# Kernel optimization log

Measured on AMD Instinct MI355X. Metric: run time of the kernel, lower is better.

## Reference

```python
import jax, jax.numpy as jnp
import numpy as np
from jax import lax

TEMP = 20.0    # args.temp
ATT_WT = 0.5   # args.att_wt
EPS = 1e-12


def l2norm(x, axis):
    # torch F.normalize: x / max(||x||_2, eps)
    n = jnp.sqrt(jnp.sum(x * x, axis=axis, keepdims=True))
    return x / jnp.maximum(n, EPS)


def conv4d(x, w):
    """4D conv, padding=1, stride=1.
    x: [B,Cin,H1,W1,H2,W2], w: [Cout,Cin,3,3,3,3] -> [B,Cout,H1,W1,H2,W2].
    Decomposed as 9 fixed (di,dj) shifts over (H1,W1), each a 2D conv over (H2,W2).
    """
    B, Cin, H1, W1, H2, W2 = x.shape
    Cout = w.shape[0]
    xp = jnp.pad(x, ((0, 0), (0, 0), (1, 1), (1, 1), (0, 0), (0, 0)))
    out = jnp.zeros((B * H1 * W1, Cout, H2, W2), x.dtype)
    for di in range(3):
        for dj in range(3):
            xs = xp[:, :, di:di + H1, dj:dj + W1]                      # [B,Cin,H1,W1,H2,W2]
            xr = xs.transpose(0, 2, 3, 1, 4, 5).reshape(B * H1 * W1, Cin, H2, W2)
            out = out + lax.conv_general_dilated(
                xr, w[:, :, di, dj], (1, 1), 'SAME',
                dimension_numbers=('NCHW', 'OIHW', 'NCHW'))
    return out.reshape(B, H1, W1, Cout, H2, W2).transpose(0, 3, 1, 2, 4, 5)


def nc_stack(x, ws):
    for w in ws:
        x = jax.nn.relu(conv4d(x, w))
    return x


def neigh_consensus(corr, ws):
    # symmetric mode: conv(C) + perm(conv(perm(C)))
    ct = corr.transpose(0, 1, 4, 5, 2, 3)
    return nc_stack(corr, ws) + nc_stack(ct, ws).transpose(0, 1, 4, 5, 2, 3)


def setup_inputs() -> dict:
    key = jax.random.key(0)
    ks = jax.random.split(key, 7)
    L, B, C, h, w = 9, 2, 1024, 20, 20
    ch = 256
    return {
        'fq_feats': jax.random.normal(ks[0], (L, B, C, h, w), jnp.float32),
        'fs_feats': jax.random.normal(ks[1], (L, B, C, h, w), jnp.float32),
        'f_q': jax.random.normal(ks[2], (B, ch, h, w), jnp.float32),
        'f_s': jax.random.normal(ks[3], (B, ch, h, w), jnp.float32),
        'w1': jax.random.normal(ks[4], (10, 9, 3, 3, 3, 3), jnp.float32) * 0.1,
        'w2': jax.random.normal(ks[5], (10, 10, 3, 3, 3, 3), jnp.float32) * 0.1,
        'w3': jax.random.normal(ks[6], (1, 10, 3, 3, 3, 3), jnp.float32) * 0.1,
    }


def reference(fq_feats, fs_feats, f_q, f_s, w1, w2, w3):
    L, B, C, h, w = fq_feats.shape
    ch = f_q.shape[1]
    hw = h * w
    # per-level channel-wise L2 normalization -> cosine correlation volume
    fqn = l2norm(fq_feats, axis=2)
    fsn = l2norm(fs_feats, axis=2)
    # corr4d[b,l,i,j,k,m] = <fq[:, i,j], fs[:, k,m]>  -> [B, L, h, w, h, w]
    corr4d = jnp.einsum('lbcij,lbckm->blijkm', fqn, fsn)
    # neighbourhood-consensus matching net -> [B,1,h,w,h,w]
    c4 = neigh_consensus(corr4d, (w1, w2, w3))
    attn = jax.nn.softmax(c4.reshape(B, hw, hw) * TEMP, axis=-1)  # over support positions
    v = f_s.reshape(B, ch, hw)
    att_fq = jnp.einsum('bqs,bcs->bcq', attn, v).reshape(B, ch, h, w)
    fq = l2norm(f_q, axis=1) + l2norm(att_fq, axis=1) * ATT_WT
    return (fq, att_fq)
```

## Files before the change

### kernel.cpp

```cpp
#include <hip/hip_runtime.h>
#include <math.h>
#include <stddef.h>

#define L9   9
#define NB   2
#define CF   1024
#define HW   400
#define CH   256
#define TEMPF 20.0f
#define EPSF  1e-12f

typedef _Float16 half8 __attribute__((ext_vector_type(8)));
typedef float f32x4 __attribute__((ext_vector_type(4)));
typedef unsigned short ushort_t;

__global__ __launch_bounds__(256) void norm_partial2(const float* __restrict__ fq,
                                                     const float* __restrict__ fs,
                                                     float* __restrict__ partial2) {
    int chunk = blockIdx.x, lb = blockIdx.y, t = blockIdx.z;
    int tid = threadIdx.x;
    if (tid >= 200) return;
    int half = tid / 100, p4 = tid - half * 100;
    const float* src = (t == 0 ? fq : fs) + (size_t)lb * CF * HW + p4 * 4;
    int c0 = chunk * 64 + half;
    f32x4 acc = {};
    #pragma unroll 8
    for (int it = 0; it < 32; ++it) {
        const float4 v = *(const float4*)(src + (size_t)(c0 + it * 2) * HW);
        acc[0] = fmaf(v.x, v.x, acc[0]);
        acc[1] = fmaf(v.y, v.y, acc[1]);
        acc[2] = fmaf(v.z, v.z, acc[2]);
        acc[3] = fmaf(v.w, v.w, acc[3]);
    }
    float* dst = partial2 + ((size_t)((t * 18 + lb) * 32) + chunk * 2 + half) * HW + p4 * 4;
    *(f32x4*)dst = acc;
}

__global__ __launch_bounds__(256) void norm_finalize2(const float* __restrict__ partial2,
                                                      float* __restrict__ invn) {
    int idx = blockIdx.x * 256 + threadIdx.x;
    if (idx >= 2 * 18 * HW) return;
    int t_lb = idx / HW;
    int ij = idx - t_lb * HW;
    const float* p = partial2 + (size_t)t_lb * 32 * HW + ij;
    float ss = 0.f;
    #pragma unroll
    for (int c = 0; c < 32; ++c) ss += p[c * HW];
    invn[idx] = 1.0f / fmaxf(sqrtf(ss), EPSF);
}

__global__ __launch_bounds__(256) void transpose_f16(const float* __restrict__ fq,
                                                     const float* __restrict__ fs,
                                                     ushort_t* __restrict__ At,
                                                     ushort_t* __restrict__ Bt,
                                                     int lb_base) {
    __shared__ float tile[64][65];
    int z = blockIdx.z;
    int tsel = z / 9, li = z - tsel * 9;
    int lb = lb_base + li;
    const float* src = (tsel ? fs : fq) + (size_t)lb * CF * HW;
    ushort_t* dst = (tsel ? Bt : At) + (size_t)li * HW * CF;
    int c0 = blockIdx.x * 64, ij0 = blockIdx.y * 64;
    int tid = threadIdx.x;
    int cl = tid >> 6;
    int col = tid & 63;
    #pragma unroll
    for (int rr = 0; rr < 16; ++rr) {
        int c_local = rr * 4 + cl;
        int ij = ij0 + col;
        tile[c_local][col] = (ij < HW) ? src[(size_t)(c0 + c_local) * HW + ij] : 0.f;
    }
    __syncthreads();
    int cp = (tid & 31) * 2;
    int rowsel = tid >> 5;
    #pragma unroll
    for (int rr = 0; rr < 8; ++rr) {
        int ij_local = rr * 8 + rowsel;
        int ij = ij0 + ij_local;
        if (ij < HW) {
            union { _Float16 h; ushort_t u; } h0, h1;
            h0.h = (_Float16)tile[cp][ij_local];
            h1.h = (_Float16)tile[cp + 1][ij_local];
            ushort2 o; o.x = h0.u; o.y = h1.u;
            *(ushort2*)(dst + (size_t)ij * CF + c0 + cp) = o;
        }
    }
}

__global__ __launch_bounds__(256) void corr_gemm_mfma(const ushort_t* __restrict__ At,
                                                      const ushort_t* __restrict__ Bt,
                                                      const float* __restrict__ invn,
                                                      ushort_t* __restrict__ corr,
                                                      int lb_base) {
    __shared__ ushort_t As[64][72];
    __shared__ ushort_t Bs[64][72];
    int li = blockIdx.z, lb = lb_base + li;
    int l = lb >> 1, b = lb & 1;
    int i0 = blockIdx.y * 64, j0 = blockIdx.x * 64;
    int tid = threadIdx.x, lane = tid & 63, w = tid >> 6;
    int mw = (w >> 1) * 32, nw = (w & 1) * 32;
    f32x4 acc[2][2] = {};
    const ushort_t* Abase = At + (size_t)li * HW * CF;
    const ushort_t* Bbase = Bt + (size_t)li * HW * CF;

    for (int kt = 0; kt < 16; ++kt) {
        int c0 = kt * 64;
        __syncthreads();
        #pragma unroll
        for (int p = 0; p < 2; ++p) {
            int idx = tid + p * 256;
            int row = idx >> 3, c8 = idx & 7;
            uint4 va = make_uint4(0, 0, 0, 0), vb = make_uint4(0, 0, 0, 0);
            if (i0 + row < HW) va = *(const uint4*)(Abase + (size_t)(i0 + row) * CF + c0 + c8 * 8);
            if (j0 + row < HW) vb = *(const uint4*)(Bbase + (size_t)(j0 + row) * CF + c0 + c8 * 8);
            *(uint4*)&As[row][c8 * 8] = va;
            *(uint4*)&Bs[row][c8 * 8] = vb;
        }
        __syncthreads();
        #pragma unroll
        for (int ks = 0; ks < 2; ++ks) {
            int k0 = ks * 32 + (lane >> 4) * 8;
            half8 a0 = *(const half8*)&As[mw + (lane & 15)][k0];
            half8 a1 = *(const half8*)&As[mw + 16 + (lane & 15)][k0];
            half8 b0 = *(const half8*)&Bs[nw + (lane & 15)][k0];
            half8 b1 = *(const half8*)&Bs[nw + 16 + (lane & 15)][k0];
            acc[0][0] = __builtin_amdgcn_mfma_f32_16x16x32_f16(a0, b0, acc[0][0], 0, 0, 0);
            acc[0][1] = __builtin_amdgcn_mfma_f32_16x16x32_f16(a0, b1, acc[0][1], 0, 0, 0);
            acc[1][0] = __builtin_amdgcn_mfma_f32_16x16x32_f16(a1, b0, acc[1][0], 0, 0, 0);
            acc[1][1] = __builtin_amdgcn_mfma_f32_16x16x32_f16(a1, b1, acc[1][1], 0, 0, 0);
        }
    }
    int obase = (b * 9 + l) * HW;
    #pragma unroll
    for (int mi = 0; mi < 2; ++mi) {
        #pragma unroll
        for (int ni = 0; ni < 2; ++ni) {
            #pragma unroll
            for (int r = 0; r < 4; ++r) {
                int ij = i0 + mw + mi * 16 + (lane >> 4) * 4 + r;
                int km = j0 + nw + ni * 16 + (lane & 15);
                if (ij < HW && km < HW) {
                    union { _Float16 h; ushort_t u; } cv;
                    cv.h = (_Float16)(acc[mi][ni][r] * invn[lb * HW + ij] * invn[7200 + lb * HW + km]);
                    corr[(size_t)(obase + ij) * HW + km] = cv.u;
                }
            }
        }
    }
}

template <int CIN, int COUT, bool SWAP>
__global__ __launch_bounds__(256) void wprep7(const float* __restrict__ wt,
                                              ushort_t* __restrict__ wb) {
    constexpr int S = CIN * 9;
    constexpr int NCH = (S + 31) / 32;
    int idx = blockIdx.x * 256 + threadIdx.x;
    int total = NCH * 4608;
    if (idx >= total) return;
    int k = idx & 31, n = (idx >> 5) & 15, dd = (idx >> 9) % 9, ch = idx / 4608;
    int slot = ch * 32 + k;
    float v = 0.f;
    if (n < COUT && slot < S) {
        int ci = slot / 9, pl = slot - ci * 9;
        int di = pl / 3, dj = pl % 3, dk = dd / 3, dm = dd % 3;
        int widx = SWAP ? ((((n * CIN + ci) * 3 + dk) * 3 + dm) * 3 + di) * 3 + dj
                        : ((((n * CIN + ci) * 3 + di) * 3 + dj) * 3 + dk) * 3 + dm;
        v = wt[widx];
    }
    union { _Float16 h; ushort_t u; } cv; cv.h = (_Float16)v;
    wb[idx] = cv.u;
}

template <int CIN, int COUT, bool DUAL, bool OUTF16>
__global__ __launch_bounds__(256) void conv4d_v8(const ushort_t* __restrict__ inA,
                                                 const ushort_t* __restrict__ inB,
                                                 const ushort_t* __restrict__ wbA,
                                                 const ushort_t* __restrict__ wbB,
                                                 void* __restrict__ outA,
                                                 void* __restrict__ outB) {
    constexpr int S = CIN * 9;
    constexpr int NCH = (S + 31) / 32;
    __shared__ __align__(16) ushort_t Ah[484 * 40];
    const int b = blockIdx.y, ij = blockIdx.x;
    const int z = blockIdx.z;
    const ushort_t* in = (DUAL || z == 0) ? inA : inB;
    const ushort_t* wbS = (DUAL || z == 0) ? wbA : wbB;
    void* outS = (DUAL || z == 0) ? outA : outB;
    const int i = ij / 20, j = ij - (ij / 20) * 20;
    const int tid = threadIdx.x, wv = tid >> 6, lane = tid & 63;
    const int m16 = lane & 15, q4 = lane >> 4;

    for (int p = tid; p < 484 * 20; p += 256) ((uint*)Ah)[p] = 0;

    int baseh[7];
    #pragma unroll
    for (int s = 0; s < 7; ++s) {
        int t = wv + 4 * s;
        if (t < 25) {
            int km = t * 16 + m16;
            int kk = km / 20, mm = km - kk * 20;
            baseh[s] = (kk * 22 + mm) * 40 + q4 * 8;
        } else baseh[s] = 0;
    }
    f32x4 accA[7] = {};
    f32x4 accB[7] = {};

    const bool stager = tid < 200;
    const int km1 = 2 * tid;
    const int r1 = stager ? ((km1 / 20 + 1) * 22 + (km1 % 20) + 1) : 0;
    int hofs[9]; bool vld[9];
    #pragma unroll
    for (int pl = 0; pl < 9; ++pl) {
        int ii = i + pl / 3 - 1, jj = j + pl % 3 - 1;
        vld[pl] = (unsigned)ii < 20u && (unsigned)jj < 20u;
        hofs[pl] = (ii * 20 + jj) * HW + km1;
    }
    const ushort_t* in_b = in + (size_t)b * CIN * HW * HW;
    const int wbase = m16 * 32 + q4 * 8;

    uint pf[32];
    #pragma unroll
    for (int u = 0; u < 32; ++u) {
        int slot = u;
        if (slot < S) {
            int ci = slot / 9, pl = slot - ci * 9;
            pf[u] = (stager && vld[pl]) ? *(const uint*)(in_b + ci * (HW * HW) + hofs[pl]) : 0u;
        } else pf[u] = 0u;
    }
    __syncthreads();

    #pragma unroll
    for (int ch = 0; ch < NCH; ++ch) {
        if (stager) {
            #pragma unroll
            for (int g4 = 0; g4 < 8; ++g4) {
                uint lo0 = (pf[4 * g4] & 0xFFFFu) | (pf[4 * g4 + 1] << 16);
                uint lo1 = (pf[4 * g4 + 2] & 0xFFFFu) | (pf[4 * g4 + 3] << 16);
                uint hi0 = (pf[4 * g4] >> 16) | (pf[4 * g4 + 1] & 0xFFFF0000u);
                uint hi1 = (pf[4 * g4 + 2] >> 16) | (pf[4 * g4 + 3] & 0xFFFF0000u);
                uint2 wlo; wlo.x = lo0; wlo.y = lo1;
                uint2 whi; whi.x = hi0; whi.y = hi1;
                *(uint2*)&Ah[(size_t)r1 * 40 + 4 * g4] = wlo;
                *(uint2*)&Ah[(size_t)(r1 + 1) * 40 + 4 * g4] = whi;
            }
        }
        __syncthreads();
        if (ch + 1 < NCH) {
            #pragma unroll
            for (int u = 0; u < 32; ++u) {
                int slot = (ch + 1) * 32 + u;
                if (slot < S) {
                    int ci = slot / 9, pl = slot - ci * 9;
                    pf[u] = (stager && vld[pl]) ? *(const uint*)(in_b + ci * (HW * HW) + hofs[pl]) : 0u;
                } else pf[u] = 0u;
            }
        }
        #pragma unroll
        for (int dd = 0; dd < 9; ++dd) {
            half8 bfA = *(const half8*)(wbS + (ch * 9 + dd) * 512 + wbase);
            half8 bfB;
            if (DUAL) bfB = *(const half8*)(wbB + (ch * 9 + dd) * 512 + wbase);
            const int doff = ((dd / 3) * 22 + (dd % 3)) * 40;
            #pragma unroll
            for (int s = 0; s < 7; ++s) {
                if (wv + 4 * s < 25) {
                    half8 af = *(const half8*)(Ah + baseh[s] + doff);
                    accA[s] = __builtin_amdgcn_mfma_f32_16x16x32_f16(af, bfA, accA[s], 0, 0, 0);
                    if (DUAL) accB[s] = __builtin_amdgcn_mfma_f32_16x16x32_f16(af, bfB, accB[s], 0, 0, 0);
                }
            }
        }
        if (ch + 1 < NCH) __syncthreads();
    }

    const int co = m16;
    if (co < COUT) {
        #pragma unroll
        for (int s = 0; s < 7; ++s) {
            int t = wv + 4 * s;
            if (t < 25) {
                int km0 = t * 16 + q4 * 4;
                size_t o = ((size_t)(b * COUT + co) * HW + ij) * HW + km0;
                if (OUTF16) {
                    union { ushort_t us[4]; uint2 u2; } pk;
                    #pragma unroll
                    for (int r = 0; r < 4; ++r) {
                        union { _Float16 h; ushort_t u16; } cv;
                        cv.h = (_Float16)fmaxf(accA[s][r], 0.f);
                        pk.us[r] = cv.u16;
                    }
                    *(uint2*)((ushort_t*)outS + o) = pk.u2;
                    if (DUAL) {
                        #pragma unroll
                        for (int r = 0; r < 4; ++r) {
                            union { _Float16 h; ushort_t u16; } cv;
                            cv.h = (_Float16)fmaxf(accB[s][r], 0.f);
                            pk.us[r] = cv.u16;
                        }
                        *(uint2*)((ushort_t*)outB + o) = pk.u2;
                    }
                } else {
                    float* op = (float*)outS + o;
                    #pragma unroll
                    for (int r = 0; r < 4; ++r)
                        op[r] = fmaxf(accA[s][r], 0.f);
                }
            }
        }
    }
}

__global__ __launch_bounds__(256) void fs_prep(const float* __restrict__ f_s,
                                               ushort_t* __restrict__ fsh) {
    int idx = blockIdx.x * 256 + threadIdx.x;
    if (idx >= NB * CH * 416) return;
    int s = idx % 416, bc = idx / 416;
    float v = (s < HW) ? f_s[(size_t)bc * HW + s] : 0.f;
    union { _Float16 h; ushort_t u; } cv; cv.h = (_Float16)v;
    fsh[idx] = cv.u;
}

__global__ __launch_bounds__(256) void softmax_av_mfma2(const float* __restrict__ c4A,
                                                        const float* __restrict__ c4B,
                                                        const ushort_t* __restrict__ fsh,
                                                        float* __restrict__ att) {
    __shared__ ushort_t P[64 * 424];
    __shared__ float invl[64];
    const int b = blockIdx.z, qb = blockIdx.x * 64;
    const int tid = threadIdx.x, wv = tid >> 6, lane = tid & 63;
    const int m16 = lane & 15, q4 = lane >> 4;
    const int lane16 = lane & 15, rg4 = lane >> 4;

    #pragma unroll 1
    for (int rg = 0; rg < 4; ++rg) {
        const int ql = wv * 16 + rg * 4 + rg4;
        int q = qb + ql; if (q > HW - 1) q = HW - 1;
        const float* rowA = c4A + ((size_t)b * HW + q) * HW;
        const float* rowB = c4B + ((size_t)b * HW + q) * HW;
        float4 v4[7];
        #pragma unroll
        for (int k4 = 0; k4 < 6; ++k4) {
            float4 a4 = *(const float4*)(rowA + 64 * k4 + lane16 * 4);
            float4 b4 = *(const float4*)(rowB + 64 * k4 + lane16 * 4);
            v4[k4] = make_float4(a4.x + b4.x, a4.y + b4.y, a4.z + b4.z, a4.w + b4.w);
        }
        if (lane16 < 4) {
            float4 a4 = *(const float4*)(rowA + 384 + lane16 * 4);
            float4 b4 = *(const float4*)(rowB + 384 + lane16 * 4);
            v4[6] = make_float4(a4.x + b4.x, a4.y + b4.y, a4.z + b4.z, a4.w + b4.w);
        } else {
            v4[6] = make_float4(-1e30f, -1e30f, -1e30f, -1e30f);
        }
        float mx = -1e30f;
        #pragma unroll
        for (int k4 = 0; k4 < 7; ++k4)
            mx = fmaxf(mx, fmaxf(fmaxf(v4[k4].x, v4[k4].y), fmaxf(v4[k4].z, v4[k4].w)));
        #pragma unroll
        for (int off = 8; off; off >>= 1) mx = fmaxf(mx, __shfl_xor(mx, off, 16));
        float sum = 0.f;
        #pragma unroll
        for (int k4 = 0; k4 < 7; ++k4) {
            if (k4 == 6 && lane16 >= 4) break;
            float e0 = __expf(TEMPF * (v4[k4].x - mx));
            float e1 = __expf(TEMPF * (v4[k4].y - mx));
            float e2 = __expf(TEMPF * (v4[k4].z - mx));
            float e3 = __expf(TEMPF * (v4[k4].w - mx));
            sum += e0 + e1 + e2 + e3;
            union { ushort_t us[4]; uint2 u2; } pk;
            union { _Float16 h; ushort_t u16; } cv;
            cv.h = (_Float16)e0; pk.us[0] = cv.u16;
            cv.h = (_Float16)e1; pk.us[1] = cv.u16;
            cv.h = (_Float16)e2; pk.us[2] = cv.u16;
            cv.h = (_Float16)e3; pk.us[3] = cv.u16;
            *(uint2*)&P[(size_t)ql * 424 + 64 * k4 + lane16 * 4] = pk.u2;
        }
        if (lane16 >= 4 && lane16 < 10) {
            uint2 z2; z2.x = 0; z2.y = 0;
            *(uint2*)&P[(size_t)ql * 424 + 384 + lane16 * 4] = z2;
        }
        #pragma unroll
        for (int off = 8; off; off >>= 1) sum += __shfl_xor(sum, off, 16);
        if (lane16 == 0) invl[ql] = 1.0f / sum;
    }

    half8 afr[13];
    #pragma unroll
    for (int ks = 0; ks < 13; ++ks)
        afr[ks] = *(const half8*)&P[(size_t)(wv * 16 + m16) * 424 + ks * 32 + q4 * 8];
    const ushort_t* fb = fsh + (size_t)b * CH * 416;
    #pragma unroll
    for (int ntl = 0; ntl < 2; ++ntl) {
        const int nt = blockIdx.y * 2 + ntl;
        const int c = nt * 16 + m16;
        const ushort_t* fc = fb + (size_t)c * 416 + q4 * 8;
        f32x4 acc = {};
        #pragma unroll
        for (int ks = 0; ks < 13; ++ks) {
            half8 bf = *(const half8*)(fc + ks * 32);
            acc = __builtin_amdgcn_mfma_f32_16x16x32_f16(afr[ks], bf, acc, 0, 0, 0);
        }
        #pragma unroll
        for (int r = 0; r < 4; ++r) {
            int ql = wv * 16 + q4 * 4 + r;
            int q = qb + ql;
            if (q < HW)
                att[((size_t)b * CH + c) * HW + q] = acc[r] * invl[ql];
        }
    }
}

__global__ __launch_bounds__(256) void final_fq(const float* __restrict__ f_q,
                                                const float* __restrict__ att,
                                                float* __restrict__ out_fq) {
    __shared__ float red[256];
    int b = blockIdx.y, q = blockIdx.x;
    int tid = threadIdx.x;
    size_t idx = (size_t)(b * CH + tid) * HW + q;
    float f = f_q[idx];
    float a = att[idx];
    red[tid] = f * f;
    __syncthreads();
    for (int s = 128; s > 0; s >>= 1) {
        if (tid < s) red[tid] += red[tid + s];
        __syncthreads();
    }
    float invf = 1.0f / fmaxf(sqrtf(red[0]), EPSF);
    __syncthreads();
    red[tid] = a * a;
    __syncthreads();
    for (int s = 128; s > 0; s >>= 1) {
        if (tid < s) red[tid] += red[tid + s];
        __syncthreads();
    }
    float inva = 1.0f / fmaxf(sqrtf(red[0]), EPSF);
    out_fq[idx] = f * invf + 0.5f * a * inva;
}

extern "C" void kernel_launch(void* const* d_in, const int* in_sizes, int n_in,
                              void* d_out, int out_size, void* d_ws, size_t ws_size,
                              hipStream_t stream) {
    const float* fq_feats = (const float*)d_in[0];
    const float* fs_feats = (const float*)d_in[1];
    const float* f_q      = (const float*)d_in[2];
    const float* f_s      = (const float*)d_in[3];
    const float* w1       = (const float*)d_in[4];
    const float* w2       = (const float*)d_in[5];
    const float* w3       = (const float*)d_in[6];
    float* out = (float*)d_out;

    float* ws      = (float*)d_ws;
    float* wbuf    = ws;
    float* invn    = wbuf + 115200;
    float* corr    = invn + 14400;
    float* buf1    = corr + 2880000;
    float* buf2    = buf1 + 3200000;
    float* att     = out + 204800;

    float* partial2 = buf1;
    ushort_t* corr_h = (ushort_t*)corr;
    ushort_t* fsh    = (ushort_t*)(corr + 1440000);
    float* c4A = corr + 1600000;
    float* c4B = corr + 1920000;
    ushort_t* At = (ushort_t*)buf1;
    ushort_t* Bt = (ushort_t*)buf2;
    ushort_t* b1A = (ushort_t*)buf1;
    ushort_t* b1B = b1A + 3200000;
    ushort_t* b2A = (ushort_t*)buf2;
    ushort_t* b2B = b2A + 3200000;

    ushort_t* wb0   = (ushort_t*)wbuf;
    ushort_t* wbL1A = wb0;
    ushort_t* wbL1B = wb0 + 13824;
    ushort_t* wbL2A = wb0 + 27648;
    ushort_t* wbL2B = wb0 + 41472;
    ushort_t* wbL3A = wb0 + 55296;
    ushort_t* wbL3B = wb0 + 69120;

    norm_partial2<<<dim3(16, 18, 2), 256, 0, stream>>>(fq_feats, fs_feats, partial2);
    norm_finalize2<<<(2 * 18 * HW + 255) / 256, 256, 0, stream>>>(partial2, invn);

    wprep7<9, 10, false><<<54, 256, 0, stream>>>(w1, wbL1A);
    wprep7<9, 10, true ><<<54, 256, 0, stream>>>(w1, wbL1B);
    wprep7<10, 10, false><<<54, 256, 0, stream>>>(w2, wbL2A);
    wprep7<10, 10, true ><<<54, 256, 0, stream>>>(w2, wbL2B);
    wprep7<10, 1, false><<<54, 256, 0, stream>>>(w3, wbL3A);
    wprep7<10, 1, true ><<<54, 256, 0, stream>>>(w3, wbL3B);
    fs_prep<<<(NB * CH * 416 + 255) / 256, 256, 0, stream>>>(f_s, fsh);

    for (int half = 0; half < 2; ++half) {
        int base = half * 9;
        transpose_f16<<<dim3(16, 7, 18), 256, 0, stream>>>(fq_feats, fs_feats, At, Bt, base);
        corr_gemm_mfma<<<dim3(7, 7, 9), 256, 0, stream>>>(At, Bt, invn, corr_h, base);
    }

    conv4d_v8<9, 10, true, true><<<dim3(400, NB, 1), 256, 0, stream>>>(
        corr_h, corr_h, wbL1A, wbL1B, b1A, b1B);
    conv4d_v8<10, 10, false, true><<<dim3(400, NB, 2), 256, 0, stream>>>(
        b1A, b1B, wbL2A, wbL2B, b2A, b2B);
    conv4d_v8<10, 1, false, false><<<dim3(400, NB, 2), 256, 0, stream>>>(
        b2A, b2B, wbL3A, wbL3B, c4A, c4B);

    softmax_av_mfma2<<<dim3(7, 8, NB), 256, 0, stream>>>(c4A, c4B, fsh, att);
    final_fq<<<dim3(400, NB), 256, 0, stream>>>(f_q, att, out);

    (void)in_sizes; (void)n_in; (void)out_size; (void)ws_size;
}
```

Measured before the change: 360.0 us.

## Double conv4d block size to 512 threads and widen LDS/output stores

The conv4d kernel now runs with 512 threads (8 waves), so each wave handles at most 4 of the 25 output M-tiles instead of 7. Wave-to-tile assignment is reversed (wt = 7 - wv), so the staging waves carry less MFMA work. LDS staging writes go from uint2 to uint4, and the fp32 final output is written as one 16-byte vector store. The changes aim to raise parallelism and cut per-wave serial MFMA work, at the cost of more waves waiting at the same barriers and higher register pressure under launch_bounds(512,5).

```diff
diff --git a/kernel.cpp b/kernel.cpp
--- a/kernel.cpp
+++ b/kernel.cpp
@@ -172,12 +172,12 @@
 }
 
 template <int CIN, int COUT, bool DUAL, bool OUTF16>
-__global__ __launch_bounds__(256) void conv4d_v8(const ushort_t* __restrict__ inA,
-                                                 const ushort_t* __restrict__ inB,
-                                                 const ushort_t* __restrict__ wbA,
-                                                 const ushort_t* __restrict__ wbB,
-                                                 void* __restrict__ outA,
-                                                 void* __restrict__ outB) {
+__global__ __launch_bounds__(512, 5) void conv4d_v9(const ushort_t* __restrict__ inA,
+                                                    const ushort_t* __restrict__ inB,
+                                                    const ushort_t* __restrict__ wbA,
+                                                    const ushort_t* __restrict__ wbB,
+                                                    void* __restrict__ outA,
+                                                    void* __restrict__ outB) {
     constexpr int S = CIN * 9;
     constexpr int NCH = (S + 31) / 32;
     __shared__ __align__(16) ushort_t Ah[484 * 40];
@@ -189,21 +189,22 @@
     const int i = ij / 20, j = ij - (ij / 20) * 20;
     const int tid = threadIdx.x, wv = tid >> 6, lane = tid & 63;
     const int m16 = lane & 15, q4 = lane >> 4;
-
-    for (int p = tid; p < 484 * 20; p += 256) ((uint*)Ah)[p] = 0;
-
-    int baseh[7];
-    #pragma unroll
-    for (int s = 0; s < 7; ++s) {
-        int t = wv + 4 * s;
+    const int wt = 7 - wv;
+
+    for (int p = tid; p < 484 * 20; p += 512) ((uint*)Ah)[p] = 0;
+
+    int baseh[4];
+    #pragma unroll
+    for (int s = 0; s < 4; ++s) {
+        int t = wt + 8 * s;
         if (t < 25) {
             int km = t * 16 + m16;
             int kk = km / 20, mm = km - kk * 20;
             baseh[s] = (kk * 22 + mm) * 40 + q4 * 8;
         } else baseh[s] = 0;
     }
-    f32x4 accA[7] = {};
-    f32x4 accB[7] = {};
+    f32x4 accA[4] = {};
+    f32x4 accB[4] = {};
 
     const bool stager = tid < 200;
     const int km1 = 2 * tid;
@@ -233,15 +234,18 @@
     for (int ch = 0; ch < NCH; ++ch) {
         if (stager) {
             #pragma unroll
-            for (int g4 = 0; g4 < 8; ++g4) {
-                uint lo0 = (pf[4 * g4] & 0xFFFFu) | (pf[4 * g4 + 1] << 16);
-                uint lo1 = (pf[4 * g4 + 2] & 0xFFFFu) | (pf[4 * g4 + 3] << 16);
-                uint hi0 = (pf[4 * g4] >> 16) | (pf[4 * g4 + 1] & 0xFFFF0000u);
-                uint hi1 = (pf[4 * g4 + 2] >> 16) | (pf[4 * g4 + 3] & 0xFFFF0000u);
-                uint2 wlo; wlo.x = lo0; wlo.y = lo1;
-                uint2 whi; whi.x = hi0; whi.y = hi1;
-                *(uint2*)&Ah[(size_t)r1 * 40 + 4 * g4] = wlo;
-                *(uint2*)&Ah[(size_t)(r1 + 1) * 40 + 4 * g4] = whi;
+            for (int g8 = 0; g8 < 4; ++g8) {
+                uint4 wlo, whi;
+                wlo.x = (pf[8 * g8 + 0] & 0xFFFFu) | (pf[8 * g8 + 1] << 16);
+                wlo.y = (pf[8 * g8 + 2] & 0xFFFFu) | (pf[8 * g8 + 3] << 16);
+                wlo.z = (pf[8 * g8 + 4] & 0xFFFFu) | (pf[8 * g8 + 5] << 16);
+                wlo.w = (pf[8 * g8 + 6] & 0xFFFFu) | (pf[8 * g8 + 7] << 16);
+                whi.x = (pf[8 * g8 + 0] >> 16) | (pf[8 * g8 + 1] & 0xFFFF0000u);
+                whi.y = (pf[8 * g8 + 2] >> 16) | (pf[8 * g8 + 3] & 0xFFFF0000u);
+                whi.z = (pf[8 * g8 + 4] >> 16) | (pf[8 * g8 + 5] & 0xFFFF0000u);
+                whi.w = (pf[8 * g8 + 6] >> 16) | (pf[8 * g8 + 7] & 0xFFFF0000u);
+                *(uint4*)&Ah[(size_t)r1 * 40 + 8 * g8] = wlo;
+                *(uint4*)&Ah[(size_t)(r1 + 1) * 40 + 8 * g8] = whi;
             }
         }
         __syncthreads();
@@ -262,8 +266,8 @@
             if (DUAL) bfB = *(const half8*)(wbB + (ch * 9 + dd) * 512 + wbase);
             const int doff = ((dd / 3) * 22 + (dd % 3)) * 40;
             #pragma unroll
-            for (int s = 0; s < 7; ++s) {
-                if (wv + 4 * s < 25) {
+            for (int s = 0; s < 4; ++s) {
+                if (wt + 8 * s < 25) {
                     half8 af = *(const half8*)(Ah + baseh[s] + doff);
                     accA[s] = __builtin_amdgcn_mfma_f32_16x16x32_f16(af, bfA, accA[s], 0, 0, 0);
                     if (DUAL) accB[s] = __builtin_amdgcn_mfma_f32_16x16x32_f16(af, bfB, accB[s], 0, 0, 0);
@@ -276,8 +280,8 @@
     const int co = m16;
     if (co < COUT) {
         #pragma unroll
-        for (int s = 0; s < 7; ++s) {
-            int t = wv + 4 * s;
+        for (int s = 0; s < 4; ++s) {
+            int t = wt + 8 * s;
             if (t < 25) {
                 int km0 = t * 16 + q4 * 4;
                 size_t o = ((size_t)(b * COUT + co) * HW + ij) * HW + km0;
@@ -300,10 +304,10 @@
                         *(uint2*)((ushort_t*)outB + o) = pk.u2;
                     }
                 } else {
-                    float* op = (float*)outS + o;
+                    f32x4 ov;
                     #pragma unroll
-                    for (int r = 0; r < 4; ++r)
-                        op[r] = fmaxf(accA[s][r], 0.f);
+                    for (int r = 0; r < 4; ++r) ov[r] = fmaxf(accA[s][r], 0.f);
+                    *(f32x4*)((float*)outS + o) = ov;
                 }
             }
         }
@@ -493,11 +497,11 @@
         corr_gemm_mfma<<<dim3(7, 7, 9), 256, 0, stream>>>(At, Bt, invn, corr_h, base);
     }
 
-    conv4d_v8<9, 10, true, true><<<dim3(400, NB, 1), 256, 0, stream>>>(
+    conv4d_v9<9, 10, true, true><<<dim3(400, NB, 1), 512, 0, stream>>>(
         corr_h, corr_h, wbL1A, wbL1B, b1A, b1B);
-    conv4d_v8<10, 10, false, true><<<dim3(400, NB, 2), 256, 0, stream>>>(
+    conv4d_v9<10, 10, false, true><<<dim3(400, NB, 2), 512, 0, stream>>>(
         b1A, b1B, wbL2A, wbL2B, b2A, b2B);
-    conv4d_v8<10, 1, false, false><<<dim3(400, NB, 2), 256, 0, stream>>>(
+    conv4d_v9<10, 1, false, false><<<dim3(400, NB, 2), 512, 0, stream>>>(
         b2A, b2B, wbL3A, wbL3B, c4A, c4B);
 
     softmax_av_mfma2<<<dim3(7, 8, NB), 256, 0, stream>>>(c4A, c4B, fsh, att);
```

Result: slower. 369.4 us (+2.6%).

## Double-buffer conv4d LDS staging so the next chunk is written during MFMA

Applied to the files above, without the earlier changes.

The conv4d kernel's shared-memory tile is widened to hold two 32-slot channel chunks, and the loop now stages chunk ch+1 into the alternate half after computing on chunk ch. This removes one of the two block barriers per chunk iteration. Only the padding border rows are zeroed instead of the whole buffer, and LDS writes are widened to 16-byte stores, as is the fp32 output store. The trade-off is that LDS use grows from about 39 KB to about 70 KB per block, which may reduce the number of resident blocks per CU.

```diff
diff --git a/kernel.cpp b/kernel.cpp
--- a/kernel.cpp
+++ b/kernel.cpp
@@ -172,15 +172,15 @@
 }
 
 template <int CIN, int COUT, bool DUAL, bool OUTF16>
-__global__ __launch_bounds__(256) void conv4d_v8(const ushort_t* __restrict__ inA,
-                                                 const ushort_t* __restrict__ inB,
-                                                 const ushort_t* __restrict__ wbA,
-                                                 const ushort_t* __restrict__ wbB,
-                                                 void* __restrict__ outA,
-                                                 void* __restrict__ outB) {
+__global__ __launch_bounds__(256) void conv4d_v12(const ushort_t* __restrict__ inA,
+                                                  const ushort_t* __restrict__ inB,
+                                                  const ushort_t* __restrict__ wbA,
+                                                  const ushort_t* __restrict__ wbB,
+                                                  void* __restrict__ outA,
+                                                  void* __restrict__ outB) {
     constexpr int S = CIN * 9;
     constexpr int NCH = (S + 31) / 32;
-    __shared__ __align__(16) ushort_t Ah[484 * 40];
+    __shared__ __align__(16) ushort_t Ah[484 * 72];
     const int b = blockIdx.y, ij = blockIdx.x;
     const int z = blockIdx.z;
     const ushort_t* in = (DUAL || z == 0) ? inA : inB;
@@ -190,7 +190,14 @@
     const int tid = threadIdx.x, wv = tid >> 6, lane = tid & 63;
     const int m16 = lane & 15, q4 = lane >> 4;
 
-    for (int p = tid; p < 484 * 20; p += 256) ((uint*)Ah)[p] = 0;
+    for (int h = tid; h < 84 * 36; h += 256) {
+        int rs = h / 36, c = h - rs * 36;
+        int row = rs < 22 ? rs
+                : rs < 44 ? 440 + rs
+                : rs < 64 ? (rs - 43) * 22
+                          : (rs - 63) * 22 + 21;
+        ((uint*)Ah)[row * 36 + c] = 0;
+    }
 
     int baseh[7];
     #pragma unroll
@@ -199,7 +206,7 @@
         if (t < 25) {
             int km = t * 16 + m16;
             int kk = km / 20, mm = km - kk * 20;
-            baseh[s] = (kk * 22 + mm) * 40 + q4 * 8;
+            baseh[s] = (kk * 22 + mm) * 72 + q4 * 8;
         } else baseh[s] = 0;
     }
     f32x4 accA[7] = {};
@@ -219,48 +226,55 @@
     const int wbase = m16 * 32 + q4 * 8;
 
     uint pf[32];
-    #pragma unroll
-    for (int u = 0; u < 32; ++u) {
-        int slot = u;
-        if (slot < S) {
-            int ci = slot / 9, pl = slot - ci * 9;
-            pf[u] = (stager && vld[pl]) ? *(const uint*)(in_b + ci * (HW * HW) + hofs[pl]) : 0u;
-        } else pf[u] = 0u;
-    }
+
+#define PFLOAD(CHV)                                                            \
+    do {                                                                       \
+        _Pragma("unroll")                                                      \
+        for (int u = 0; u < 32; ++u) {                                         \
+            int slot = (CHV) * 32 + u;                                         \
+            if (slot < S) {                                                    \
+                int ci = slot / 9, pl = slot - ci * 9;                         \
+                pf[u] = (stager && vld[pl])                                    \
+                        ? *(const uint*)(in_b + ci * (HW * HW) + hofs[pl])     \
+                        : 0u;                                                  \
+            } else pf[u] = 0u;                                                 \
+        }                                                                      \
+    } while (0)
+
+#define STAGE(HSEL)                                                            \
+    do {                                                                       \
+        if (stager) {                                                          \
+            _Pragma("unroll")                                                  \
+            for (int g8 = 0; g8 < 4; ++g8) {                                   \
+                uint4 wlo, whi;                                                \
+                wlo.x = (pf[8 * g8 + 0] & 0xFFFFu) | (pf[8 * g8 + 1] << 16);   \
+                wlo.y = (pf[8 * g8 + 2] & 0xFFFFu) | (pf[8 * g8 + 3] << 16);   \
+                wlo.z = (pf[8 * g8 + 4] & 0xFFFFu) | (pf[8 * g8 + 5] << 16);   \
+                wlo.w = (pf[8 * g8 + 6] & 0xFFFFu) | (pf[8 * g8 + 7] << 16);   \
+                whi.x = (pf[8 * g8 + 0] >> 16) | (pf[8 * g8 + 1] & 0xFFFF0000u);\
+                whi.y = (pf[8 * g8 + 2] >> 16) | (pf[8 * g8 + 3] & 0xFFFF0000u);\
+                whi.z = (pf[8 * g8 + 4] >> 16) | (pf[8 * g8 + 5] & 0xFFFF0000u);\
+                whi.w = (pf[8 * g8 + 6] >> 16) | (pf[8 * g8 + 7] & 0xFFFF0000u);\
+                *(uint4*)&Ah[(size_t)r1 * 72 + (HSEL) + 8 * g8] = wlo;         \
+                *(uint4*)&Ah[(size_t)(r1 + 1) * 72 + (HSEL) + 8 * g8] = whi;   \
+            }                                                                  \
+        }                                                                      \
+    } while (0)
+
+    PFLOAD(0);
+    STAGE(0);
     __syncthreads();
 
     #pragma unroll
     for (int ch = 0; ch < NCH; ++ch) {
-        if (stager) {
-            #pragma unroll
-            for (int g4 = 0; g4 < 8; ++g4) {
-                uint lo0 = (pf[4 * g4] & 0xFFFFu) | (pf[4 * g4 + 1] << 16);
-                uint lo1 = (pf[4 * g4 + 2] & 0xFFFFu) | (pf[4 * g4 + 3] << 16);
-                uint hi0 = (pf[4 * g4] >> 16) | (pf[4 * g4 + 1] & 0xFFFF0000u);
-                uint hi1 = (pf[4 * g4 + 2] >> 16) | (pf[4 * g4 + 3] & 0xFFFF0000u);
-                uint2 wlo; wlo.x = lo0; wlo.y = lo1;
-                uint2 whi; whi.x = hi0; whi.y = hi1;
-                *(uint2*)&Ah[(size_t)r1 * 40 + 4 * g4] = wlo;
-                *(uint2*)&Ah[(size_t)(r1 + 1) * 40 + 4 * g4] = whi;
-            }
-        }
-        __syncthreads();
-        if (ch + 1 < NCH) {
-            #pragma unroll
-            for (int u = 0; u < 32; ++u) {
-                int slot = (ch + 1) * 32 + u;
-                if (slot < S) {
-                    int ci = slot / 9, pl = slot - ci * 9;
-                    pf[u] = (stager && vld[pl]) ? *(const uint*)(in_b + ci * (HW * HW) + hofs[pl]) : 0u;
-                } else pf[u] = 0u;
-            }
-        }
+        if (ch + 1 < NCH) PFLOAD(ch + 1);
+        const int hsel = (ch & 1) * 32;
         #pragma unroll
         for (int dd = 0; dd < 9; ++dd) {
             half8 bfA = *(const half8*)(wbS + (ch * 9 + dd) * 512 + wbase);
             half8 bfB;
             if (DUAL) bfB = *(const half8*)(wbB + (ch * 9 + dd) * 512 + wbase);
-            const int doff = ((dd / 3) * 22 + (dd % 3)) * 40;
+            const int doff = ((dd / 3) * 22 + (dd % 3)) * 72 + hsel;
             #pragma unroll
             for (int s = 0; s < 7; ++s) {
                 if (wv + 4 * s < 25) {
@@ -270,8 +284,13 @@
                 }
             }
         }
-        if (ch + 1 < NCH) __syncthreads();
-    }
+        if (ch + 1 < NCH) {
+            STAGE(((ch + 1) & 1) * 32);
+            __syncthreads();
+        }
+    }
+#undef PFLOAD
+#undef STAGE
 
     const int co = m16;
     if (co < COUT) {
@@ -300,10 +319,10 @@
                         *(uint2*)((ushort_t*)outB + o) = pk.u2;
                     }
                 } else {
-                    float* op = (float*)outS + o;
+                    f32x4 ov;
                     #pragma unroll
-                    for (int r = 0; r < 4; ++r)
-                        op[r] = fmaxf(accA[s][r], 0.f);
+                    for (int r = 0; r < 4; ++r) ov[r] = fmaxf(accA[s][r], 0.f);
+                    *(f32x4*)((float*)outS + o) = ov;
                 }
             }
         }
@@ -493,11 +512,11 @@
         corr_gemm_mfma<<<dim3(7, 7, 9), 256, 0, stream>>>(At, Bt, invn, corr_h, base);
     }
 
-    conv4d_v8<9, 10, true, true><<<dim3(400, NB, 1), 256, 0, stream>>>(
+    conv4d_v12<9, 10, true, true><<<dim3(400, NB, 1), 256, 0, stream>>>(
         corr_h, corr_h, wbL1A, wbL1B, b1A, b1B);
-    conv4d_v8<10, 10, false, true><<<dim3(400, NB, 2), 256, 0, stream>>>(
+    conv4d_v12<10, 10, false, true><<<dim3(400, NB, 2), 256, 0, stream>>>(
         b1A, b1B, wbL2A, wbL2B, b2A, b2B);
-    conv4d_v8<10, 1, false, false><<<dim3(400, NB, 2), 256, 0, stream>>>(
+    conv4d_v12<10, 1, false, false><<<dim3(400, NB, 2), 256, 0, stream>>>(
         b2A, b2B, wbL3A, wbL3B, c4A, c4B);
 
     softmax_av_mfma2<<<dim3(7, 8, NB), 256, 0, stream>>>(c4A, c4B, fsh, att);
```

Result: slower. 385.3 us (+7.0%).

## Compute two adjacent output positions per block in conv4d layers two and three

Applied to the files above, without the earlier changes.

Layers two and three of the 4D convolution now compute two neighbouring (i,j) output positions per block. The block stages a 3x4 neighbourhood of input slices (12 planes per channel instead of 9), so shifted copies of the weights let both outputs share the staged data. For the single-output-channel layer 3, both positions are packed into two columns of one MFMA, which removes the wasted 15 of 16 output columns. The aim is fewer global loads per output and better MFMA utilization, in exchange for a larger reduction dimension (12/9 more K work) and half as many blocks.

```diff
diff --git a/kernel.cpp b/kernel.cpp
--- a/kernel.cpp
+++ b/kernel.cpp
@@ -171,21 +171,45 @@
     wb[idx] = cv.u;
 }
 
-template <int CIN, int COUT, bool DUAL, bool OUTF16>
-__global__ __launch_bounds__(256) void conv4d_v8(const ushort_t* __restrict__ inA,
-                                                 const ushort_t* __restrict__ inB,
+template <int CIN, int COUT, bool SWAP, int MODE>
+__global__ __launch_bounds__(256) void wprep12(const float* __restrict__ wt,
+                                               ushort_t* __restrict__ wb) {
+    constexpr int S2 = CIN * 12;
+    constexpr int NCH = (S2 + 31) / 32;
+    int idx = blockIdx.x * 256 + threadIdx.x;
+    int total = NCH * 4608;
+    if (idx >= total) return;
+    int k = idx & 31, n = (idx >> 5) & 15, dd = (idx >> 9) % 9, ch = idx / 4608;
+    int slot = ch * 32 + k;
+    float v = 0.f;
+    if (slot < S2) {
+        int ci = slot / 12, r = slot - ci * 12;
+        int di = r >> 2, dj4 = r & 3;
+        int dk = dd / 3, dm = dd % 3;
+        int off = (MODE == 2) ? n : MODE;
+        int e = dj4 - off;
+        int nn = (MODE == 2) ? 0 : n;
+        bool ok = (MODE == 2) ? (n < 2) : (n < COUT);
+        if (ok && e >= 0 && e <= 2) {
+            int widx = SWAP ? ((((nn * CIN + ci) * 3 + dk) * 3 + dm) * 3 + di) * 3 + e
+                            : ((((nn * CIN + ci) * 3 + di) * 3 + e) * 3 + dk) * 3 + dm;
+            v = wt[widx];
+        }
+    }
+    union { _Float16 h; ushort_t u; } cv; cv.h = (_Float16)v;
+    wb[idx] = cv.u;
+}
+
+template <int CIN, int COUT>
+__global__ __launch_bounds__(256) void conv4d_l1(const ushort_t* __restrict__ in,
                                                  const ushort_t* __restrict__ wbA,
                                                  const ushort_t* __restrict__ wbB,
-                                                 void* __restrict__ outA,
-                                                 void* __restrict__ outB) {
+                                                 ushort_t* __restrict__ outA,
+                                                 ushort_t* __restrict__ outB) {
     constexpr int S = CIN * 9;
     constexpr int NCH = (S + 31) / 32;
     __shared__ __align__(16) ushort_t Ah[484 * 40];
     const int b = blockIdx.y, ij = blockIdx.x;
-    const int z = blockIdx.z;
-    const ushort_t* in = (DUAL || z == 0) ? inA : inB;
-    const ushort_t* wbS = (DUAL || z == 0) ? wbA : wbB;
-    void* outS = (DUAL || z == 0) ? outA : outB;
     const int i = ij / 20, j = ij - (ij / 20) * 20;
     const int tid = threadIdx.x, wv = tid >> 6, lane = tid & 63;
     const int m16 = lane & 15, q4 = lane >> 4;
@@ -257,16 +281,15 @@
         }
         #pragma unroll
         for (int dd = 0; dd < 9; ++dd) {
-            half8 bfA = *(const half8*)(wbS + (ch * 9 + dd) * 512 + wbase);
-            half8 bfB;
-            if (DUAL) bfB = *(const half8*)(wbB + (ch * 9 + dd) * 512 + wbase);
+            half8 bfA = *(const half8*)(wbA + (ch * 9 + dd) * 512 + wbase);
+            half8 bfB = *(const half8*)(wbB + (ch * 9 + dd) * 512 + wbase);
             const int doff = ((dd / 3) * 22 + (dd % 3)) * 40;
             #pragma unroll
             for (int s = 0; s < 7; ++s) {
                 if (wv + 4 * s < 25) {
                     half8 af = *(const half8*)(Ah + baseh[s] + doff);
                     accA[s] = __builtin_amdgcn_mfma_f32_16x16x32_f16(af, bfA, accA[s], 0, 0, 0);
-                    if (DUAL) accB[s] = __builtin_amdgcn_mfma_f32_16x16x32_f16(af, bfB, accB[s], 0, 0, 0);
+                    accB[s] = __builtin_amdgcn_mfma_f32_16x16x32_f16(af, bfB, accB[s], 0, 0, 0);
                 }
             }
         }
@@ -281,29 +304,180 @@
             if (t < 25) {
                 int km0 = t * 16 + q4 * 4;
                 size_t o = ((size_t)(b * COUT + co) * HW + ij) * HW + km0;
-                if (OUTF16) {
-                    union { ushort_t us[4]; uint2 u2; } pk;
+                union { ushort_t us[4]; uint2 u2; } pk;
+                #pragma unroll
+                for (int r = 0; r < 4; ++r) {
+                    union { _Float16 h; ushort_t u16; } cv;
+                    cv.h = (_Float16)fmaxf(accA[s][r], 0.f);
+                    pk.us[r] = cv.u16;
+                }
+                *(uint2*)(outA + o) = pk.u2;
+                #pragma unroll
+                for (int r = 0; r < 4; ++r) {
+                    union { _Float16 h; ushort_t u16; } cv;
+                    cv.h = (_Float16)fmaxf(accB[s][r], 0.f);
+                    pk.us[r] = cv.u16;
+                }
+                *(uint2*)(outB + o) = pk.u2;
+            }
+        }
+    }
+}
+
+template <int CIN, int COUT, bool MERGED, bool OUTF16>
+__global__ __launch_bounds__(256) void conv4d_2ij(
+        const ushort_t* __restrict__ inA, const ushort_t* __restrict__ inB,
+        const ushort_t* __restrict__ wA1, const ushort_t* __restrict__ wA2,
+        const ushort_t* __restrict__ wB1, const ushort_t* __restrict__ wB2,
+        void* __restrict__ outA, void* __restrict__ outB) {
+    constexpr int S2 = CIN * 12;
+    constexpr int NCH = (S2 + 31) / 32;
+    __shared__ __align__(16) ushort_t Ah[484 * 40];
+    const int b = blockIdx.y, bx = blockIdx.x, z = blockIdx.z;
+    const ushort_t* in = z ? inB : inA;
+    const ushort_t* w1 = z ? wB1 : wA1;
+    const ushort_t* w2 = z ? wB2 : wA2;
+    void* outS = z ? outB : outA;
+    const int i = bx / 10, jp = bx - (bx / 10) * 10;
+    const int j0 = 2 * jp;
+    const int ij0 = i * 20 + j0;
+    const int tid = threadIdx.x, wv = tid >> 6, lane = tid & 63;
+    const int m16 = lane & 15, q4 = lane >> 4;
+
+    for (int p = tid; p < 484 * 20; p += 256) ((uint*)Ah)[p] = 0;
+
+    int baseh[7];
+    #pragma unroll
+    for (int s = 0; s < 7; ++s) {
+        int t = wv + 4 * s;
+        if (t < 25) {
+            int km = t * 16 + m16;
+            int kk = km / 20, mm = km - kk * 20;
+            baseh[s] = (kk * 22 + mm) * 40 + q4 * 8;
+        } else baseh[s] = 0;
+    }
+    f32x4 acc1[7] = {};
+    f32x4 acc2[7] = {};
+
+    const bool stager = tid < 200;
+    const int km1 = 2 * tid;
+    const int r1 = stager ? ((km1 / 20 + 1) * 22 + (km1 % 20) + 1) : 0;
+    int hofs[12]; bool vld[12];
+    #pragma unroll
+    for (int pl = 0; pl < 12; ++pl) {
+        int di = pl >> 2, dj = pl & 3;
+        int ii = i + di - 1, jj = j0 + dj - 1;
+        vld[pl] = (unsigned)ii < 20u && (unsigned)jj < 20u;
+        hofs[pl] = (ii * 20 + jj) * HW + km1;
+    }
+    const ushort_t* in_b = in + (size_t)b * CIN * HW * HW;
+    const int wbase = m16 * 32 + q4 * 8;
+
+    uint pf[32];
+    #pragma unroll
+    for (int u = 0; u < 32; ++u) {
+        int slot = u;
+        if (slot < S2) {
+            int ci = slot / 12, pl = slot - ci * 12;
+            pf[u] = (stager && vld[pl]) ? *(const uint*)(in_b + ci * (HW * HW) + hofs[pl]) : 0u;
+        } else pf[u] = 0u;
+    }
+    __syncthreads();
+
+    #pragma unroll
+    for (int ch = 0; ch < NCH; ++ch) {
+        if (stager) {
+            #pragma unroll
+            for (int g4 = 0; g4 < 8; ++g4) {
+                uint lo0 = (pf[4 * g4] & 0xFFFFu) | (pf[4 * g4 + 1] << 16);
+                uint lo1 = (pf[4 * g4 + 2] & 0xFFFFu) | (pf[4 * g4 + 3] << 16);
+                uint hi0 = (pf[4 * g4] >> 16) | (pf[4 * g4 + 1] & 0xFFFF0000u);
+                uint hi1 = (pf[4 * g4 + 2] >> 16) | (pf[4 * g4 + 3] & 0xFFFF0000u);
+                uint2 wlo; wlo.x = lo0; wlo.y = lo1;
+                uint2 whi; whi.x = hi0; whi.y = hi1;
+                *(uint2*)&Ah[(size_t)r1 * 40 + 4 * g4] = wlo;
+                *(uint2*)&Ah[(size_t)(r1 + 1) * 40 + 4 * g4] = whi;
+            }
+        }
+        __syncthreads();
+        if (ch + 1 < NCH) {
+            #pragma unroll
+            for (int u = 0; u < 32; ++u) {
+                int slot = (ch + 1) * 32 + u;
+                if (slot < S2) {
+                    int ci = slot / 12, pl = slot - ci * 12;
+                    pf[u] = (stager && vld[pl]) ? *(const uint*)(in_b + ci * (HW * HW) + hofs[pl]) : 0u;
+                } else pf[u] = 0u;
+            }
+        }
+        #pragma unroll
+        for (int dd = 0; dd < 9; ++dd) {
+            half8 bf1 = *(const half8*)(w1 + (ch * 9 + dd) * 512 + wbase);
+            half8 bf2;
+            if (!MERGED) bf2 = *(const half8*)(w2 + (ch * 9 + dd) * 512 + wbase);
+            const int doff = ((dd / 3) * 22 + (dd % 3)) * 40;
+            #pragma unroll
+            for (int s = 0; s < 7; ++s) {
+                if (wv + 4 * s < 25) {
+                    half8 af = *(const half8*)(Ah + baseh[s] + doff);
+                    acc1[s] = __builtin_amdgcn_mfma_f32_16x16x32_f16(af, bf1, acc1[s], 0, 0, 0);
+                    if (!MERGED) acc2[s] = __builtin_amdgcn_mfma_f32_16x16x32_f16(af, bf2, acc2[s], 0, 0, 0);
+                }
+            }
+        }
+        if (ch + 1 < NCH) __syncthreads();
+    }
+
+    if (MERGED) {
+        if (m16 < 2) {
+            const int ij = ij0 + m16;
+            #pragma unroll
+            for (int s = 0; s < 7; ++s) {
+                int t = wv + 4 * s;
+                if (t < 25) {
+                    int km0 = t * 16 + q4 * 4;
+                    size_t o = ((size_t)b * HW + ij) * HW + km0;
+                    f32x4 ov;
                     #pragma unroll
-                    for (int r = 0; r < 4; ++r) {
-                        union { _Float16 h; ushort_t u16; } cv;
-                        cv.h = (_Float16)fmaxf(accA[s][r], 0.f);
-                        pk.us[r] = cv.u16;
-                    }
-                    *(uint2*)((ushort_t*)outS + o) = pk.u2;
-                    if (DUAL) {
+                    for (int r = 0; r < 4; ++r) ov[r] = fmaxf(acc1[s][r], 0.f);
+                    *(f32x4*)((float*)outS + o) = ov;
+                }
+            }
+        }
+    } else {
+        const int co = m16;
+        if (co < COUT) {
+            #pragma unroll
+            for (int s = 0; s < 7; ++s) {
+                int t = wv + 4 * s;
+                if (t < 25) {
+                    int km0 = t * 16 + q4 * 4;
+                    size_t o = ((size_t)(b * COUT + co) * HW + ij0) * HW + km0;
+                    if (OUTF16) {
+                        union { ushort_t us[4]; uint2 u2; } pk;
                         #pragma unroll
                         for (int r = 0; r < 4; ++r) {
                             union { _Float16 h; ushort_t u16; } cv;
-                            cv.h = (_Float16)fmaxf(accB[s][r], 0.f);
+                            cv.h = (_Float16)fmaxf(acc1[s][r], 0.f);
                             pk.us[r] = cv.u16;
                         }
-                        *(uint2*)((ushort_t*)outB + o) = pk.u2;
+                        *(uint2*)((ushort_t*)outS + o) = pk.u2;
+                        #pragma unroll
+                        for (int r = 0; r < 4; ++r) {
+                            union { _Float16 h; ushort_t u16; } cv;
+                            cv.h = (_Float16)fmaxf(acc2[s][r], 0.f);
+                            pk.us[r] = cv.u16;
+                        }
+                        *(uint2*)((ushort_t*)outS + o + HW) = pk.u2;
+                    } else {
+                        f32x4 ov;
+                        #pragma unroll
+                        for (int r = 0; r < 4; ++r) ov[r] = fmaxf(acc1[s][r], 0.f);
+                        *(f32x4*)((float*)outS + o) = ov;
+                        #pragma unroll
+                        for (int r = 0; r < 4; ++r) ov[r] = fmaxf(acc2[s][r], 0.f);
+                        *(f32x4*)((float*)outS + o + HW) = ov;
                     }
-                } else {
-                    float* op = (float*)outS + o;
-                    #pragma unroll
-                    for (int r = 0; r < 4; ++r)
-                        op[r] = fmaxf(accA[s][r], 0.f);
                 }
             }
         }
@@ -468,23 +642,27 @@
     ushort_t* b2A = (ushort_t*)buf2;
     ushort_t* b2B = b2A + 3200000;
 
-    ushort_t* wb0   = (ushort_t*)wbuf;
-    ushort_t* wbL1A = wb0;
-    ushort_t* wbL1B = wb0 + 13824;
-    ushort_t* wbL2A = wb0 + 27648;
-    ushort_t* wbL2B = wb0 + 41472;
-    ushort_t* wbL3A = wb0 + 55296;
-    ushort_t* wbL3B = wb0 + 69120;
+    ushort_t* wb0    = (ushort_t*)wbuf;
+    ushort_t* wbL1A  = wb0;
+    ushort_t* wbL1B  = wb0 + 13824;
+    ushort_t* wbL2A0 = wb0 + 27648;
+    ushort_t* wbL2A1 = wb0 + 46080;
+    ushort_t* wbL2B0 = wb0 + 64512;
+    ushort_t* wbL2B1 = wb0 + 82944;
+    ushort_t* wbL3Am = wb0 + 101376;
+    ushort_t* wbL3Bm = wb0 + 119808;
 
     norm_partial2<<<dim3(16, 18, 2), 256, 0, stream>>>(fq_feats, fs_feats, partial2);
     norm_finalize2<<<(2 * 18 * HW + 255) / 256, 256, 0, stream>>>(partial2, invn);
 
     wprep7<9, 10, false><<<54, 256, 0, stream>>>(w1, wbL1A);
     wprep7<9, 10, true ><<<54, 256, 0, stream>>>(w1, wbL1B);
-    wprep7<10, 10, false><<<54, 256, 0, stream>>>(w2, wbL2A);
-    wprep7<10, 10, true ><<<54, 256, 0, stream>>>(w2, wbL2B);
-    wprep7<10, 1, false><<<54, 256, 0, stream>>>(w3, wbL3A);
-    wprep7<10, 1, true ><<<54, 256, 0, stream>>>(w3, wbL3B);
+    wprep12<10, 10, false, 0><<<72, 256, 0, stream>>>(w2, wbL2A0);
+    wprep12<10, 10, false, 1><<<72, 256, 0, stream>>>(w2, wbL2A1);
+    wprep12<10, 10, true,  0><<<72, 256, 0, stream>>>(w2, wbL2B0);
+    wprep12<10, 10, true,  1><<<72, 256, 0, stream>>>(w2, wbL2B1);
+    wprep12<10, 1, false, 2><<<72, 256, 0, stream>>>(w3, wbL3Am);
+    wprep12<10, 1, true,  2><<<72, 256, 0, stream>>>(w3, wbL3Bm);
     fs_prep<<<(NB * CH * 416 + 255) / 256, 256, 0, stream>>>(f_s, fsh);
 
     for (int half = 0; half < 2; ++half) {
@@ -493,12 +671,12 @@
         corr_gemm_mfma<<<dim3(7, 7, 9), 256, 0, stream>>>(At, Bt, invn, corr_h, base);
     }
 
-    conv4d_v8<9, 10, true, true><<<dim3(400, NB, 1), 256, 0, stream>>>(
-        corr_h, corr_h, wbL1A, wbL1B, b1A, b1B);
-    conv4d_v8<10, 10, false, true><<<dim3(400, NB, 2), 256, 0, stream>>>(
-        b1A, b1B, wbL2A, wbL2B, b2A, b2B);
-    conv4d_v8<10, 1, false, false><<<dim3(400, NB, 2), 256, 0, stream>>>(
-        b2A, b2B, wbL3A, wbL3B, c4A, c4B);
+    conv4d_l1<9, 10><<<dim3(400, NB, 1), 256, 0, stream>>>(
+        corr_h, wbL1A, wbL1B, b1A, b1B);
+    conv4d_2ij<10, 10, false, true><<<dim3(200, NB, 2), 256, 0, stream>>>(
+        b1A, b1B, wbL2A0, wbL2A1, wbL2B0, wbL2B1, b2A, b2B);
+    conv4d_2ij<10, 1, true, false><<<dim3(200, NB, 2), 256, 0, stream>>>(
+        b2A, b2B, wbL3Am, wbL3Am, wbL3Bm, wbL3Bm, c4A, c4B);
 
     softmax_av_mfma2<<<dim3(7, 8, NB), 256, 0, stream>>>(c4A, c4B, fsh, att);
     final_fq<<<dim3(400, NB), 256, 0, stream>>>(f_q, att, out);
```

Result: no change. 364.4 us (+1.2%).
